# Kernel optimization log

Hardware: AMD Instinct MI355X
Metric: run time of the kernel (lower is better)

## Reference

```python
import jax, jax.numpy as jnp
import numpy as np

B, N, HID = 32768, 27, 128
SINKHORN_ITERS = 20
LN_EPS = 1e-5


def _layer_norm(x, g, b):
    mu = jnp.mean(x, axis=-1, keepdims=True)
    var = jnp.mean((x - mu) ** 2, axis=-1, keepdims=True)
    return (x - mu) * jax.lax.rsqrt(var + LN_EPS) * g + b


def setup_inputs() -> dict:
    key = jax.random.key(0)
    ks = jax.random.split(key, 6)
    A = jax.random.uniform(ks[0], (B, N, N), dtype=jnp.float32)
    m = jax.random.normal(ks[1], (B, N), dtype=jnp.float32)
    tau_r = jnp.ones((), dtype=jnp.float32)
    # MLP params: LayerNorm(4) -> Linear(4,128) -> ReLU -> Linear(128,128) -> LayerNorm(128)
    ln1_g = jnp.ones((4,), jnp.float32)
    ln1_b = jnp.zeros((4,), jnp.float32)
    W1 = jax.random.normal(ks[2], (4, HID), dtype=jnp.float32) * 0.1
    b1 = jnp.zeros((HID,), jnp.float32)
    W2 = jax.random.normal(ks[3], (HID, HID), dtype=jnp.float32) * 0.05
    b2 = jnp.zeros((HID,), jnp.float32)
    ln2_g = jnp.ones((HID,), jnp.float32)
    ln2_b = jnp.zeros((HID,), jnp.float32)
    protos = jax.random.normal(ks[4], (N, HID), dtype=jnp.float32) * 0.02
    return {"A": A, "m": m, "tau_r": tau_r, "ln1_g": ln1_g, "ln1_b": ln1_b,
            "W1": W1, "b1": b1, "W2": W2, "b2": b2,
            "ln2_g": ln2_g, "ln2_b": ln2_b, "protos": protos}


def reference(A, m, tau_r, ln1_g, ln1_b, W1, b1, W2, b2, ln2_g, ln2_b, protos):
    # ---- feature build: [log1p(rowsum), top1_offdiag, top2_offdiag, m] ----
    row_sum = jnp.sum(A, axis=-1)                       # (B,N)
    eye = jnp.eye(N, dtype=A.dtype)
    offdiag = A * (1.0 - eye)                           # (B,N,N)
    top2_vals, _ = jax.lax.top_k(offdiag, 2)            # (B,N,2)
    feat = jnp.stack([jnp.log1p(row_sum), top2_vals[..., 0], top2_vals[..., 1], m], axis=-1)  # (B,N,4)
    # ---- MLP: LN -> Linear -> ReLU -> (Dropout=id) -> Linear -> LN ----
    h = _layer_norm(feat, ln1_g, ln1_b)
    h = jax.nn.relu(h @ W1 + b1)
    h = h @ W2 + b2
    H = _layer_norm(h, ln2_g, ln2_b)                    # (B,N,HID)
    # ---- scores vs slot prototypes, transposed, temperature ----
    scores = jnp.einsum('bnh,kh->bnk', H, protos)       # (B,N,N)
    log_alpha = jnp.swapaxes(scores, 1, 2) / tau_r
    # ---- log-domain Sinkhorn, 20 iterations ----
    def body(_, la):
        la = la - jax.nn.logsumexp(la, axis=-1, keepdims=True)
        la = la - jax.nn.logsumexp(la, axis=-2, keepdims=True)
        return la
    log_alpha = jax.lax.fori_loop(0, SINKHORN_ITERS, body, log_alpha)
    return jnp.exp(log_alpha)                           # (B,N,N) soft permutation R_L
```

## Files before the change

kernel.cpp:

```cpp
#include <hip/hip_runtime.h>
#include <math.h>

#define NN 27
#define HID 128
#define SITERS 20
#define H1S 136

typedef float    v4    __attribute__((ext_vector_type(4)));
typedef _Float16 f16x8 __attribute__((ext_vector_type(8)));

__global__ void k0_prep(const float* __restrict__ W2, const float* __restrict__ protos,
                        _Float16* __restrict__ Bsw, _Float16* __restrict__ Asw)
{
    int t0 = blockIdx.x * 256 + threadIdx.x;
    for (int idx = t0; idx < 4*8*64*8; idx += 8*256) {
        int j = idx & 7, l = (idx >> 3) & 63, nt = (idx >> 9) & 7, kt = idx >> 12;
        int k = kt*32 + (l >> 4)*8 + j, n = nt*16 + (l & 15);
        Bsw[idx] = (_Float16)W2[k*HID + n];
    }
    for (int idx = t0; idx < 2*4*64*8; idx += 8*256) {
        int j = idx & 7, l = (idx >> 3) & 63, kt = (idx >> 9) & 3, mt = idx >> 11;
        int k = kt*32 + (l >> 4)*8 + j, mm = mt*16 + (l & 15);
        Asw[idx] = (mm < NN) ? (_Float16)protos[mm*HID + k] : (_Float16)0.0f;
    }
}

__global__ __launch_bounds__(128, 8) void k1_mlp(
    const float* __restrict__ A, const float* __restrict__ m,
    const float* __restrict__ tau_r,
    const float* __restrict__ ln1g, const float* __restrict__ ln1b,
    const float* __restrict__ W1, const float* __restrict__ b1,
    const float* __restrict__ b2,
    const float* __restrict__ ln2g, const float* __restrict__ ln2b,
    const _Float16* __restrict__ Bsw, const _Float16* __restrict__ Asw,
    float* __restrict__ out)
{
    __shared__ __align__(16) _Float16 sBuf[32 * H1S];
    __shared__ __align__(16) float    sFeat[NN*4 + 4];

    float*    sA   = (float*)sBuf;
    _Float16* sH1  = sBuf;
    _Float16* sH   = sBuf;
    float*    part = (float*)sBuf;

    const int b   = blockIdx.x;
    const int tid = threadIdx.x;
    const int l = tid & 63, w = tid >> 6;
    const int c = l & 15, g = l >> 4;
    const float* Ab = A + (size_t)b * (NN * NN);

    for (int i = tid; i < NN * NN; i += 128) sA[i] = Ab[i];
    __syncthreads();

    if (tid < NN) {
        const int n = tid;
        float sum = 0.f, m1 = -1e30f, m2 = -1e30f;
        #pragma unroll
        for (int j = 0; j < NN; ++j) {
            float a = sA[n * NN + j];
            sum += a;
            float v = (j == n) ? 0.f : a;
            float nm1 = fmaxf(m1, v);
            m2 = fmaxf(m2, fminf(m1, v));
            m1 = nm1;
        }
        float f0 = log1pf(sum), f1 = m1, f2 = m2, f3 = m[(size_t)b * NN + n];
        float mu = 0.25f * (f0 + f1 + f2 + f3);
        float d0 = f0 - mu, d1 = f1 - mu, d2 = f2 - mu, d3 = f3 - mu;
        float var = 0.25f * (d0*d0 + d1*d1 + d2*d2 + d3*d3);
        float rs  = rsqrtf(var + 1e-5f);
        sFeat[n*4 + 0] = d0 * rs * ln1g[0] + ln1b[0];
        sFeat[n*4 + 1] = d1 * rs * ln1g[1] + ln1b[1];
        sFeat[n*4 + 2] = d2 * rs * ln1g[2] + ln1b[2];
        sFeat[n*4 + 3] = d3 * rs * ln1g[3] + ln1b[3];
    }
    __syncthreads();

    {
        const float w0 = W1[tid], w1 = W1[HID + tid], w2 = W1[2*HID + tid], w3 = W1[3*HID + tid];
        const float bb = b1[tid];
        #pragma unroll 9
        for (int n = 0; n < NN; ++n) {
            v4 f = *(const v4*)&sFeat[n * 4];
            float v = fmaf(f[0], w0, fmaf(f[1], w1, fmaf(f[2], w2, fmaf(f[3], w3, bb))));
            sH1[n * H1S + tid] = (_Float16)fmaxf(v, 0.f);
        }
        #pragma unroll
        for (int n = NN; n < 32; ++n) sH1[n * H1S + tid] = (_Float16)0.f;
    }
    __syncthreads();

    f16x8 af[4];
    #pragma unroll
    for (int kt = 0; kt < 4; ++kt)
        af[kt] = *(const f16x8*)&sH1[(w*16 + c) * H1S + kt*32 + g*8];

    const f16x8* Bv = (const f16x8*)Bsw;

    float s4[4]  = {0.f, 0.f, 0.f, 0.f};
    float ss4[4] = {0.f, 0.f, 0.f, 0.f};
    #pragma unroll 1
    for (int nt = 0; nt < 8; ++nt) {
        v4 a = (v4)(0.f);
        #pragma unroll
        for (int kt = 0; kt < 4; ++kt)
            a = __builtin_amdgcn_mfma_f32_16x16x32_f16(af[kt], Bv[(kt*8 + nt)*64 + l], a, 0, 0, 0);
        float b2v = b2[nt*16 + c];
        #pragma unroll
        for (int r = 0; r < 4; ++r) {
            float v = a[r] + b2v;
            s4[r] += v; ss4[r] += v * v;
        }
    }
    float muv[4], rsv[4];
    #pragma unroll
    for (int r = 0; r < 4; ++r) {
        #pragma unroll
        for (int mask = 1; mask <= 8; mask <<= 1) {
            s4[r]  += __shfl_xor(s4[r],  mask);
            ss4[r] += __shfl_xor(ss4[r], mask);
        }
        float mu  = s4[r] * (1.0f / HID);
        float var = ss4[r] * (1.0f / HID) - mu * mu;
        muv[r] = mu;
        rsv[r] = rsqrtf(var + 1e-5f);
    }

    #pragma unroll 1
    for (int nt = 0; nt < 8; ++nt) {
        v4 a = (v4)(0.f);
        #pragma unroll
        for (int kt = 0; kt < 4; ++kt)
            a = __builtin_amdgcn_mfma_f32_16x16x32_f16(af[kt], Bv[(kt*8 + nt)*64 + l], a, 0, 0, 0);
        int col = nt*16 + c;
        float b2v = b2[col], g2 = ln2g[col], bb = ln2b[col];
        #pragma unroll
        for (int r = 0; r < 4; ++r) {
            float hv = (a[r] + b2v - muv[r]) * rsv[r] * g2 + bb;
            sH[(w*16 + 4*g + r) * H1S + col] = (_Float16)hv;
        }
    }
    __syncthreads();

    v4 acc2[2];
    {
        const f16x8* Av = (const f16x8*)Asw;
        acc2[0] = (v4)(0.f); acc2[1] = (v4)(0.f);
        #pragma unroll
        for (int kt = 0; kt < 4; ++kt) {
            f16x8 pa  = Av[(w*4 + kt)*64 + l];
            f16x8 b0  = *(const f16x8*)&sH[(c)      * H1S + kt*32 + g*8];
            f16x8 b1f = *(const f16x8*)&sH[(16 + c) * H1S + kt*32 + g*8];
            acc2[0] = __builtin_amdgcn_mfma_f32_16x16x32_f16(pa, b0,  acc2[0], 0, 0, 0);
            acc2[1] = __builtin_amdgcn_mfma_f32_16x16x32_f16(pa, b1f, acc2[1], 0, 0, 0);
        }
    }
    __syncthreads();

    const int i0 = w*16 + 4*g;
    const int j1 = 16 + c;
    float p0[4], p1[4];
    float rowm[4], rowp[4];
    #pragma unroll
    for (int r = 0; r < 4; ++r) {
        rowm[r] = ((i0 + r) < NN) ? 1.f : 0.f;
        rowp[r] = 1.f - rowm[r];
    }
    const float colm1 = (j1 < NN) ? 1.f : 0.f;
    const float colp1 = 1.f - colm1;
    {
        const float inv_tau = 1.0f / tau_r[0];
        #pragma unroll
        for (int r = 0; r < 4; ++r) {
            bool iok = (i0 + r) < NN;
            p0[r] = iok ? __expf(acc2[0][r] * inv_tau) : 0.f;
            p1[r] = (iok && j1 < NN) ? __expf(acc2[1][r] * inv_tau) : 0.f;
        }
    }

    for (int it = 0; it < SITERS; ++it) {
        #pragma unroll
        for (int r = 0; r < 4; ++r) {
            float s = p0[r] + p1[r];
            s += __shfl_xor(s, 1);
            s += __shfl_xor(s, 2);
            s += __shfl_xor(s, 4);
            s += __shfl_xor(s, 8);
            float rho = __builtin_amdgcn_rcpf(s + rowp[r]) * rowm[r];
            p0[r] *= rho;
            p1[r] *= rho;
        }
        float t0 = (p0[0] + p0[1]) + (p0[2] + p0[3]);
        float t1 = (p1[0] + p1[1]) + (p1[2] + p1[3]);
        t0 += __shfl_xor(t0, 16);  t0 += __shfl_xor(t0, 32);
        t1 += __shfl_xor(t1, 16);  t1 += __shfl_xor(t1, 32);
        float* pb = part + (it & 1) * 64;
        if (g == 0) {
            pb[w*32 + c]      = t0;
            pb[w*32 + 16 + c] = t1;
        }
        __syncthreads();
        float cs0 = t0 + pb[(w^1)*32 + c];
        float cs1 = t1 + pb[(w^1)*32 + 16 + c];
        float rc0 = __builtin_amdgcn_rcpf(cs0);
        float rc1 = __builtin_amdgcn_rcpf(cs1 + colp1) * colm1;
        #pragma unroll
        for (int r = 0; r < 4; ++r) {
            p0[r] *= rc0;
            p1[r] *= rc1;
        }
    }

    {
        float* ob = out + (size_t)b * (NN * NN);
        #pragma unroll
        for (int r = 0; r < 4; ++r) {
            int i = i0 + r;
            if (i < NN) {
                ob[i * NN + c] = p0[r];
                if (j1 < NN) ob[i * NN + j1] = p1[r];
            }
        }
    }
}

extern "C" void kernel_launch(void* const* d_in, const int* in_sizes, int n_in,
                              void* d_out, int out_size, void* d_ws, size_t ws_size,
                              hipStream_t stream) {
    const float* A      = (const float*)d_in[0];
    const float* m      = (const float*)d_in[1];
    const float* tau_r  = (const float*)d_in[2];
    const float* ln1g   = (const float*)d_in[3];
    const float* ln1b   = (const float*)d_in[4];
    const float* W1     = (const float*)d_in[5];
    const float* b1     = (const float*)d_in[6];
    const float* W2     = (const float*)d_in[7];
    const float* b2     = (const float*)d_in[8];
    const float* ln2g   = (const float*)d_in[9];
    const float* ln2b   = (const float*)d_in[10];
    const float* protos = (const float*)d_in[11];
    float* out = (float*)d_out;

    const int B = in_sizes[0] / (NN * NN);

    _Float16* Bsw = (_Float16*)d_ws;
    _Float16* Asw = (_Float16*)((char*)d_ws + 32768);

    k0_prep<<<8, 256, 0, stream>>>(W2, protos, Bsw, Asw);
    k1_mlp<<<B, 128, 0, stream>>>(A, m, tau_r, ln1g, ln1b, W1, b1, b2,
                                  ln2g, ln2b, Bsw, Asw, out);
}
```

Measured before the change: 547.7 us.

## Use one wave per batch item to drop block barriers in Sinkhorn

Each block now runs a single 64-lane wave that handles all 32 padded rows of a batch item, instead of two waves splitting the rows. This removes every __syncthreads and the per-iteration shared-memory exchange of column partial sums in the 20 Sinkhorn iterations; column sums become pure in-wave shuffles. It also reuses each loaded W2 fragment across two M tiles. The cost is doubled register pressure per lane and fewer threads per block, with launch bounds changed to (64,4), which may limit occupancy.

```diff
diff --git a/kernel.cpp b/kernel.cpp
--- a/kernel.cpp
+++ b/kernel.cpp
@@ -25,7 +25,7 @@
     }
 }
 
-__global__ __launch_bounds__(128, 8) void k1_mlp(
+__global__ __launch_bounds__(64, 4) void k1_mlp(
     const float* __restrict__ A, const float* __restrict__ m,
     const float* __restrict__ tau_r,
     const float* __restrict__ ln1g, const float* __restrict__ ln1b,
@@ -41,19 +41,17 @@
     float*    sA   = (float*)sBuf;
     _Float16* sH1  = sBuf;
     _Float16* sH   = sBuf;
-    float*    part = (float*)sBuf;
-
-    const int b   = blockIdx.x;
-    const int tid = threadIdx.x;
-    const int l = tid & 63, w = tid >> 6;
+
+    const int b = blockIdx.x;
+    const int l = threadIdx.x;
     const int c = l & 15, g = l >> 4;
     const float* Ab = A + (size_t)b * (NN * NN);
 
-    for (int i = tid; i < NN * NN; i += 128) sA[i] = Ab[i];
-    __syncthreads();
-
-    if (tid < NN) {
-        const int n = tid;
+    for (int i = l; i < NN * NN; i += 64) sA[i] = Ab[i];
+    __builtin_amdgcn_wave_barrier();
+
+    if (l < NN) {
+        const int n = l;
         float sum = 0.f, m1 = -1e30f, m2 = -1e30f;
         #pragma unroll
         for (int j = 0; j < NN; ++j) {
@@ -74,140 +72,173 @@
         sFeat[n*4 + 2] = d2 * rs * ln1g[2] + ln1b[2];
         sFeat[n*4 + 3] = d3 * rs * ln1g[3] + ln1b[3];
     }
-    __syncthreads();
-
-    {
-        const float w0 = W1[tid], w1 = W1[HID + tid], w2 = W1[2*HID + tid], w3 = W1[3*HID + tid];
-        const float bb = b1[tid];
+    __builtin_amdgcn_wave_barrier();
+
+    {
+        const float w0a = W1[l],      w1a = W1[HID + l],      w2a = W1[2*HID + l],      w3a = W1[3*HID + l];
+        const float w0b = W1[64 + l], w1b = W1[HID + 64 + l], w2b = W1[2*HID + 64 + l], w3b = W1[3*HID + 64 + l];
+        const float bba = b1[l], bbb = b1[64 + l];
         #pragma unroll 9
         for (int n = 0; n < NN; ++n) {
             v4 f = *(const v4*)&sFeat[n * 4];
-            float v = fmaf(f[0], w0, fmaf(f[1], w1, fmaf(f[2], w2, fmaf(f[3], w3, bb))));
-            sH1[n * H1S + tid] = (_Float16)fmaxf(v, 0.f);
-        }
-        #pragma unroll
-        for (int n = NN; n < 32; ++n) sH1[n * H1S + tid] = (_Float16)0.f;
-    }
-    __syncthreads();
-
-    f16x8 af[4];
+            float va = fmaf(f[0], w0a, fmaf(f[1], w1a, fmaf(f[2], w2a, fmaf(f[3], w3a, bba))));
+            float vb = fmaf(f[0], w0b, fmaf(f[1], w1b, fmaf(f[2], w2b, fmaf(f[3], w3b, bbb))));
+            sH1[n * H1S + l]      = (_Float16)fmaxf(va, 0.f);
+            sH1[n * H1S + 64 + l] = (_Float16)fmaxf(vb, 0.f);
+        }
+        #pragma unroll
+        for (int n = NN; n < 32; ++n) {
+            sH1[n * H1S + l]      = (_Float16)0.f;
+            sH1[n * H1S + 64 + l] = (_Float16)0.f;
+        }
+    }
+    __builtin_amdgcn_wave_barrier();
+
+    f16x8 af[2][4];
     #pragma unroll
-    for (int kt = 0; kt < 4; ++kt)
-        af[kt] = *(const f16x8*)&sH1[(w*16 + c) * H1S + kt*32 + g*8];
+    for (int mt = 0; mt < 2; ++mt)
+        #pragma unroll
+        for (int kt = 0; kt < 4; ++kt)
+            af[mt][kt] = *(const f16x8*)&sH1[(mt*16 + c) * H1S + kt*32 + g*8];
 
     const f16x8* Bv = (const f16x8*)Bsw;
 
-    float s4[4]  = {0.f, 0.f, 0.f, 0.f};
-    float ss4[4] = {0.f, 0.f, 0.f, 0.f};
+    float s4[2][4]  = {{0.f,0.f,0.f,0.f},{0.f,0.f,0.f,0.f}};
+    float ss4[2][4] = {{0.f,0.f,0.f,0.f},{0.f,0.f,0.f,0.f}};
     #pragma unroll 1
     for (int nt = 0; nt < 8; ++nt) {
-        v4 a = (v4)(0.f);
-        #pragma unroll
-        for (int kt = 0; kt < 4; ++kt)
-            a = __builtin_amdgcn_mfma_f32_16x16x32_f16(af[kt], Bv[(kt*8 + nt)*64 + l], a, 0, 0, 0);
+        f16x8 bf[4];
+        #pragma unroll
+        for (int kt = 0; kt < 4; ++kt) bf[kt] = Bv[(kt*8 + nt)*64 + l];
         float b2v = b2[nt*16 + c];
         #pragma unroll
-        for (int r = 0; r < 4; ++r) {
-            float v = a[r] + b2v;
-            s4[r] += v; ss4[r] += v * v;
-        }
-    }
-    float muv[4], rsv[4];
+        for (int mt = 0; mt < 2; ++mt) {
+            v4 a = (v4)(0.f);
+            #pragma unroll
+            for (int kt = 0; kt < 4; ++kt)
+                a = __builtin_amdgcn_mfma_f32_16x16x32_f16(af[mt][kt], bf[kt], a, 0, 0, 0);
+            #pragma unroll
+            for (int r = 0; r < 4; ++r) {
+                float v = a[r] + b2v;
+                s4[mt][r] += v; ss4[mt][r] += v * v;
+            }
+        }
+    }
+    float muv[2][4], rsv[2][4];
+    #pragma unroll
+    for (int mt = 0; mt < 2; ++mt)
+        #pragma unroll
+        for (int r = 0; r < 4; ++r) {
+            #pragma unroll
+            for (int mask = 1; mask <= 8; mask <<= 1) {
+                s4[mt][r]  += __shfl_xor(s4[mt][r],  mask);
+                ss4[mt][r] += __shfl_xor(ss4[mt][r], mask);
+            }
+            float mu  = s4[mt][r] * (1.0f / HID);
+            float var = ss4[mt][r] * (1.0f / HID) - mu * mu;
+            muv[mt][r] = mu;
+            rsv[mt][r] = rsqrtf(var + 1e-5f);
+        }
+
+    #pragma unroll 1
+    for (int nt = 0; nt < 8; ++nt) {
+        f16x8 bf[4];
+        #pragma unroll
+        for (int kt = 0; kt < 4; ++kt) bf[kt] = Bv[(kt*8 + nt)*64 + l];
+        int col = nt*16 + c;
+        float b2v = b2[col], g2 = ln2g[col], bb = ln2b[col];
+        #pragma unroll
+        for (int mt = 0; mt < 2; ++mt) {
+            v4 a = (v4)(0.f);
+            #pragma unroll
+            for (int kt = 0; kt < 4; ++kt)
+                a = __builtin_amdgcn_mfma_f32_16x16x32_f16(af[mt][kt], bf[kt], a, 0, 0, 0);
+            #pragma unroll
+            for (int r = 0; r < 4; ++r) {
+                float hv = (a[r] + b2v - muv[mt][r]) * rsv[mt][r] * g2 + bb;
+                sH[(mt*16 + 4*g + r) * H1S + col] = (_Float16)hv;
+            }
+        }
+    }
+    __builtin_amdgcn_wave_barrier();
+
+    v4 acc2[2][2];
+    acc2[0][0] = (v4)(0.f); acc2[0][1] = (v4)(0.f);
+    acc2[1][0] = (v4)(0.f); acc2[1][1] = (v4)(0.f);
+    {
+        const f16x8* Av = (const f16x8*)Asw;
+        #pragma unroll
+        for (int kt = 0; kt < 4; ++kt) {
+            f16x8 b0  = *(const f16x8*)&sH[(c)      * H1S + kt*32 + g*8];
+            f16x8 b1f = *(const f16x8*)&sH[(16 + c) * H1S + kt*32 + g*8];
+            f16x8 pa0 = Av[(0*4 + kt)*64 + l];
+            f16x8 pa1 = Av[(1*4 + kt)*64 + l];
+            acc2[0][0] = __builtin_amdgcn_mfma_f32_16x16x32_f16(pa0, b0,  acc2[0][0], 0, 0, 0);
+            acc2[0][1] = __builtin_amdgcn_mfma_f32_16x16x32_f16(pa0, b1f, acc2[0][1], 0, 0, 0);
+            acc2[1][0] = __builtin_amdgcn_mfma_f32_16x16x32_f16(pa1, b0,  acc2[1][0], 0, 0, 0);
+            acc2[1][1] = __builtin_amdgcn_mfma_f32_16x16x32_f16(pa1, b1f, acc2[1][1], 0, 0, 0);
+        }
+    }
+
+    float p[2][2][4];
+    float rowm1[4], rowp1[4];
     #pragma unroll
     for (int r = 0; r < 4; ++r) {
-        #pragma unroll
-        for (int mask = 1; mask <= 8; mask <<= 1) {
-            s4[r]  += __shfl_xor(s4[r],  mask);
-            ss4[r] += __shfl_xor(ss4[r], mask);
-        }
-        float mu  = s4[r] * (1.0f / HID);
-        float var = ss4[r] * (1.0f / HID) - mu * mu;
-        muv[r] = mu;
-        rsv[r] = rsqrtf(var + 1e-5f);
-    }
-
-    #pragma unroll 1
-    for (int nt = 0; nt < 8; ++nt) {
-        v4 a = (v4)(0.f);
-        #pragma unroll
-        for (int kt = 0; kt < 4; ++kt)
-            a = __builtin_amdgcn_mfma_f32_16x16x32_f16(af[kt], Bv[(kt*8 + nt)*64 + l], a, 0, 0, 0);
-        int col = nt*16 + c;
-        float b2v = b2[col], g2 = ln2g[col], bb = ln2b[col];
-        #pragma unroll
-        for (int r = 0; r < 4; ++r) {
-            float hv = (a[r] + b2v - muv[r]) * rsv[r] * g2 + bb;
-            sH[(w*16 + 4*g + r) * H1S + col] = (_Float16)hv;
-        }
-    }
-    __syncthreads();
-
-    v4 acc2[2];
-    {
-        const f16x8* Av = (const f16x8*)Asw;
-        acc2[0] = (v4)(0.f); acc2[1] = (v4)(0.f);
-        #pragma unroll
-        for (int kt = 0; kt < 4; ++kt) {
-            f16x8 pa  = Av[(w*4 + kt)*64 + l];
-            f16x8 b0  = *(const f16x8*)&sH[(c)      * H1S + kt*32 + g*8];
-            f16x8 b1f = *(const f16x8*)&sH[(16 + c) * H1S + kt*32 + g*8];
-            acc2[0] = __builtin_amdgcn_mfma_f32_16x16x32_f16(pa, b0,  acc2[0], 0, 0, 0);
-            acc2[1] = __builtin_amdgcn_mfma_f32_16x16x32_f16(pa, b1f, acc2[1], 0, 0, 0);
-        }
-    }
-    __syncthreads();
-
-    const int i0 = w*16 + 4*g;
-    const int j1 = 16 + c;
-    float p0[4], p1[4];
-    float rowm[4], rowp[4];
-    #pragma unroll
-    for (int r = 0; r < 4; ++r) {
-        rowm[r] = ((i0 + r) < NN) ? 1.f : 0.f;
-        rowp[r] = 1.f - rowm[r];
-    }
-    const float colm1 = (j1 < NN) ? 1.f : 0.f;
+        rowm1[r] = ((16 + 4*g + r) < NN) ? 1.f : 0.f;
+        rowp1[r] = 1.f - rowm1[r];
+    }
+    const float colm1 = ((16 + c) < NN) ? 1.f : 0.f;
     const float colp1 = 1.f - colm1;
     {
         const float inv_tau = 1.0f / tau_r[0];
         #pragma unroll
         for (int r = 0; r < 4; ++r) {
-            bool iok = (i0 + r) < NN;
-            p0[r] = iok ? __expf(acc2[0][r] * inv_tau) : 0.f;
-            p1[r] = (iok && j1 < NN) ? __expf(acc2[1][r] * inv_tau) : 0.f;
+            p[0][0][r] = __expf(acc2[0][0][r] * inv_tau);
+            p[0][1][r] = (colm1 != 0.f) ? __expf(acc2[0][1][r] * inv_tau) : 0.f;
+            bool iok = (16 + 4*g + r) < NN;
+            p[1][0][r] = iok ? __expf(acc2[1][0][r] * inv_tau) : 0.f;
+            p[1][1][r] = (iok && colm1 != 0.f) ? __expf(acc2[1][1][r] * inv_tau) : 0.f;
         }
     }
 
     for (int it = 0; it < SITERS; ++it) {
         #pragma unroll
         for (int r = 0; r < 4; ++r) {
-            float s = p0[r] + p1[r];
+            float s = p[0][0][r] + p[0][1][r];
             s += __shfl_xor(s, 1);
             s += __shfl_xor(s, 2);
             s += __shfl_xor(s, 4);
             s += __shfl_xor(s, 8);
-            float rho = __builtin_amdgcn_rcpf(s + rowp[r]) * rowm[r];
-            p0[r] *= rho;
-            p1[r] *= rho;
-        }
-        float t0 = (p0[0] + p0[1]) + (p0[2] + p0[3]);
-        float t1 = (p1[0] + p1[1]) + (p1[2] + p1[3]);
+            float rho = __builtin_amdgcn_rcpf(s);
+            p[0][0][r] *= rho;
+            p[0][1][r] *= rho;
+        }
+        #pragma unroll
+        for (int r = 0; r < 4; ++r) {
+            float s = p[1][0][r] + p[1][1][r];
+            s += __shfl_xor(s, 1);
+            s += __shfl_xor(s, 2);
+            s += __shfl_xor(s, 4);
+            s += __shfl_xor(s, 8);
+            float rho = __builtin_amdgcn_rcpf(s + rowp1[r]) * rowm1[r];
+            p[1][0][r] *= rho;
+            p[1][1][r] *= rho;
+        }
+        float t0 = ((p[0][0][0] + p[0][0][1]) + (p[0][0][2] + p[0][0][3]))
+                 + ((p[1][0][0] + p[1][0][1]) + (p[1][0][2] + p[1][0][3]));
+        float t1 = ((p[0][1][0] + p[0][1][1]) + (p[0][1][2] + p[0][1][3]))
+                 + ((p[1][1][0] + p[1][1][1]) + (p[1][1][2] + p[1][1][3]));
         t0 += __shfl_xor(t0, 16);  t0 += __shfl_xor(t0, 32);
         t1 += __shfl_xor(t1, 16);  t1 += __shfl_xor(t1, 32);
-        float* pb = part + (it & 1) * 64;
-        if (g == 0) {
-            pb[w*32 + c]      = t0;
-            pb[w*32 + 16 + c] = t1;
-        }
-        __syncthreads();
-        float cs0 = t0 + pb[(w^1)*32 + c];
-        float cs1 = t1 + pb[(w^1)*32 + 16 + c];
-        float rc0 = __builtin_amdgcn_rcpf(cs0);
-        float rc1 = __builtin_amdgcn_rcpf(cs1 + colp1) * colm1;
-        #pragma unroll
-        for (int r = 0; r < 4; ++r) {
-            p0[r] *= rc0;
-            p1[r] *= rc1;
+        float rc0 = __builtin_amdgcn_rcpf(t0);
+        float rc1 = __builtin_amdgcn_rcpf(t1 + colp1) * colm1;
+        #pragma unroll
+        for (int mt = 0; mt < 2; ++mt) {
+            #pragma unroll
+            for (int r = 0; r < 4; ++r) {
+                p[mt][0][r] *= rc0;
+                p[mt][1][r] *= rc1;
+            }
         }
     }
 
@@ -215,10 +246,16 @@
         float* ob = out + (size_t)b * (NN * NN);
         #pragma unroll
         for (int r = 0; r < 4; ++r) {
-            int i = i0 + r;
+            int i = 4*g + r;
+            ob[i * NN + c] = p[0][0][r];
+            if ((16 + c) < NN) ob[i * NN + 16 + c] = p[0][1][r];
+        }
+        #pragma unroll
+        for (int r = 0; r < 4; ++r) {
+            int i = 16 + 4*g + r;
             if (i < NN) {
-                ob[i * NN + c] = p0[r];
-                if (j1 < NN) ob[i * NN + j1] = p1[r];
+                ob[i * NN + c] = p[1][0][r];
+                if ((16 + c) < NN) ob[i * NN + 16 + c] = p[1][1][r];
             }
         }
     }
@@ -247,6 +284,6 @@
     _Float16* Asw = (_Float16*)((char*)d_ws + 32768);
 
     k0_prep<<<8, 256, 0, stream>>>(W2, protos, Bsw, Asw);
-    k1_mlp<<<B, 128, 0, stream>>>(A, m, tau_r, ln1g, ln1b, W1, b1, b2,
-                                  ln2g, ln2b, Bsw, Asw, out);
+    k1_mlp<<<B, 64, 0, stream>>>(A, m, tau_r, ln1g, ln1b, W1, b1, b2,
+                                 ln2g, ln2b, Bsw, Asw, out);
 }
```

Measured after the change: 514.0 us. 1.07x faster.
